# Kernel tuning notes

Hardware: AMD Instinct MI355X
Metric: run time of the kernel (lower is better)

The kernel has to match this reference:

```python
import jax, jax.numpy as jnp
import numpy as np

SEQ, B, OBS, H, MLP_H, ACT = 64, 8192, 47, 64, 32, 12


def setup_inputs() -> dict:
    key = jax.random.key(0)
    ks = jax.random.split(key, 10)
    s = 1.0 / np.sqrt(H)
    return {
        "obs_seq": jax.random.normal(ks[0], (SEQ, B, OBS), dtype=jnp.float32),
        "h0": jnp.zeros((1, B, H), jnp.float32),
        "c0": jnp.zeros((1, B, H), jnp.float32),
        "W_ih": jax.random.uniform(ks[1], (4 * H, OBS), jnp.float32, -s, s),
        "W_hh": jax.random.uniform(ks[2], (4 * H, H), jnp.float32, -s, s),
        "b_ih": jax.random.uniform(ks[3], (4 * H,), jnp.float32, -s, s),
        "b_hh": jax.random.uniform(ks[4], (4 * H,), jnp.float32, -s, s),
        "W1": jax.random.uniform(ks[5], (MLP_H, H), jnp.float32, -s, s),
        "b1": jax.random.uniform(ks[6], (MLP_H,), jnp.float32, -s, s),
        "W2": jax.random.uniform(ks[7], (ACT, MLP_H), jnp.float32, -0.1, 0.1),
        "b2": jnp.zeros((ACT,), jnp.float32),
        "masks": jax.random.randint(ks[8], (SEQ, B), 0, 2, dtype=jnp.int32),
    }


def _lstm_scan(obs_seq, h0, c0, W_ih, W_hh, b_ih, b_hh, masks):
    b = b_ih + b_hh

    def step(carry, inp):
        h, c = carry  # (B,H)
        x, m = inp
        m = m.astype(h.dtype)[:, None]  # (B,1): 0 resets hidden state
        h = h * m
        c = c * m
        gates = x @ W_ih.T + h @ W_hh.T + b  # (B,4H), torch order i,f,g,o
        i, f, g, o = jnp.split(gates, 4, axis=-1)
        c = jax.nn.sigmoid(f) * c + jax.nn.sigmoid(i) * jnp.tanh(g)
        h = jax.nn.sigmoid(o) * jnp.tanh(c)
        return (h, c), h

    (h, c), outs = jax.lax.scan(step, (h0[0], c0[0]), (obs_seq, masks))
    return outs, h, c


def reference(obs_seq, h0, c0, W_ih, W_hh, b_ih, b_hh, W1, b1, W2, b2, masks):
    lstm_out, h, c = _lstm_scan(obs_seq, h0, c0, W_ih, W_hh, b_ih, b_hh, masks)
    means = jax.nn.elu(lstm_out @ W1.T + b1) @ W2.T + b2  # (SEQ,B,ACT)
    return means, h[None], c[None]
```

## Files before the change

### kernel.cpp

```cpp
#include <hip/hip_runtime.h>
#include <hip/hip_bf16.h>

#define SEQ   64
#define BATCH 8192
#define OBS   47
#define HID   64
#define MLPH  32
#define ACT   12

#define BT 16
#define NT 512
#define NWG (BATCH / BT)

#define XS0O 0
#define XS1O 2048
#define HM0O 4096
#define HM1O 6144
#define XA0O 8192
#define XA1O 24576
#define M2OO 40960
#define MSKO 41984
#define W1LO 46080
#define W2LO 50176
#define SMEM_BYTES 51200

#define L2E  1.4426950408889634f
#define L2E2 2.8853900817779268f

typedef __attribute__((ext_vector_type(8))) short short8;
typedef __attribute__((ext_vector_type(4))) float f32x4;

__device__ __forceinline__ ushort f2bf(float f) {
  union { float f; unsigned u; } v; v.f = f;
  return (ushort)((v.u + 0x7FFFu + ((v.u >> 16) & 1u)) >> 16);
}
__device__ __forceinline__ float ex2(float x) {
#if __has_builtin(__builtin_amdgcn_exp2f)
  return __builtin_amdgcn_exp2f(x);
#else
  return __expf(x * 0.6931471805599453f);
#endif
}
__device__ __forceinline__ float rcpx(float x) {
#if __has_builtin(__builtin_amdgcn_rcpf)
  return __builtin_amdgcn_rcpf(x);
#else
  return __fdividef(1.0f, x);
#endif
}
__device__ __forceinline__ float sigf(float x)     { return rcpx(1.0f + ex2(-L2E * x)); }
__device__ __forceinline__ float tanhfast(float x) { return __builtin_fmaf(-2.0f, rcpx(1.0f + ex2(L2E2 * x)), 1.0f); }
__device__ __forceinline__ unsigned cvtpk(float lo, float hi) {
  unsigned r; asm("v_cvt_pk_bf16_f32 %0, %1, %2" : "=v"(r) : "v"(lo), "v"(hi)); return r;
}

__device__ __forceinline__ void barrier_lgkm() {
  __builtin_amdgcn_sched_barrier(0);
  asm volatile("s_waitcnt lgkmcnt(0)" ::: "memory");
  __builtin_amdgcn_s_barrier();
  __builtin_amdgcn_sched_barrier(0);
}

__device__ __forceinline__ int swz (int r, int ks) { return (r * 128 + ks * 2) ^ ((r & 7) << 4); }
__device__ __forceinline__ int swzM(int r, int cs) { return (r * 64  + cs * 2) ^ ((r & 7) << 4); }

extern "C" __global__ void __launch_bounds__(NT, 4)
lstm_policy(const float* __restrict__ obs, const float* __restrict__ h0,
            const float* __restrict__ c0, const float* __restrict__ Wih,
            const float* __restrict__ Whh, const float* __restrict__ bih,
            const float* __restrict__ bhh, const float* __restrict__ W1,
            const float* __restrict__ b1, const float* __restrict__ W2,
            const float* __restrict__ b2, const int* __restrict__ masks,
            float* __restrict__ out)
{
  __shared__ __align__(16) char sm[SMEM_BYTES];
  const int tid  = threadIdx.x;
  const int b0   = blockIdx.x * BT;
  const int lane = tid & 63;
  const int w    = tid >> 6;
  const int lr   = lane & 15;
  const int lg   = lane >> 4;
  const int j    = (w & 3) * 16 + lr;

  int xsl[4];
  #pragma unroll
  for (int nf = 0; nf < 4; ++nf)
    xsl[nf] = (j << 8) + ((((lg * 4 + nf) ^ lr) & 15) << 4);

  for (int idx = tid; idx < 256; idx += NT)
    *(f32x4*)(sm + idx * 16) = (f32x4){0.f, 0.f, 0.f, 0.f};
  for (int idx = tid; idx < SEQ * BT; idx += NT) {
    int t = idx >> 4, r = idx & 15;
    *(float*)(sm + MSKO + idx * 4) = (float)masks[t * BATCH + b0 + r];
  }
  if (tid < 64) {
    int l = tid, llr = l & 15, llg = l >> 4;
    #pragma unroll
    for (int tt = 0; tt < 2; ++tt)
      #pragma unroll
      for (int kk = 0; kk < 2; ++kk) {
        short8 f;
        const float* src = W1 + (tt * 16 + llr) * HID + kk * 32 + llg * 8;
        #pragma unroll
        for (int e = 0; e < 8; ++e) f[e] = (short)f2bf(src[e]);
        *(short8*)(sm + W1LO + ((tt * 2 + kk) * 64 + l) * 16) = f;
      }
    short8 f2;
    #pragma unroll
    for (int e = 0; e < 8; ++e)
      f2[e] = (llr < ACT) ? (short)f2bf(W2[llr * MLPH + llg * 8 + e]) : (short)0;
    *(short8*)(sm + W2LO + l * 16) = f2;
  }
  __syncthreads();

  short8 wf[4][2];
  float biasg[4] = {0, 0, 0, 0};
  float creg[4] = {0, 0, 0, 0}, hlast[4] = {0, 0, 0, 0};
  int shw[4];
  #pragma unroll
  for (int q = 0; q < 4; ++q) shw[q] = swz(lg * 4 + q, j);

  if (w < 4) {
    #pragma unroll
    for (int nf = 0; nf < 4; ++nf) {
      int n = nf * 64 + j;
      #pragma unroll
      for (int kk = 0; kk < 2; ++kk) {
        const float* src = Whh + n * HID + kk * 32 + lg * 8;
        short8 f;
        #pragma unroll
        for (int e = 0; e < 8; ++e) f[e] = (short)f2bf(src[e]);
        wf[nf][kk] = f;
      }
    }
    #pragma unroll
    for (int q = 0; q < 4; ++q) {
      int r = lg * 4 + q;
      creg[q] = c0[(size_t)(b0 + r) * HID + j];
      *(ushort*)(sm + HM0O + shw[q]) = f2bf(h0[(size_t)(b0 + r) * HID + j]);
    }
  } else {
    #pragma unroll
    for (int nf = 0; nf < 4; ++nf) {
      int n = nf * 64 + j;
      biasg[nf] = bih[n] + bhh[n];
      #pragma unroll
      for (int kk = 0; kk < 2; ++kk) {
        short8 f;
        #pragma unroll
        for (int e = 0; e < 8; ++e) {
          int k = kk * 32 + lg * 8 + e;
          f[e] = (k < OBS) ? (short)f2bf(Wih[n * OBS + k]) : (short)0;
        }
        wf[nf][kk] = f;
      }
    }
  }

  float b1v0 = 0.f, b1v1 = 0.f, b2v = 0.f;
  float* outp = out + ((size_t)(b0 + lg * 4)) * ACT + lr;
  if (w == 4) { b1v0 = b1[lr]; b1v1 = b1[16 + lr]; b2v = (lr < ACT) ? b2[lr] : 0.f; }

  const int oidx = tid - 320;
  const bool oact = (w >= 5) && (oidx >= 0) && (oidx < 188);
  int a_obs[4] = {0, 0, 0, 0};
  f32x4 ovh = {0.f, 0.f, 0.f, 0.f};
  const float* obsp = obs;
  if (oact) {
    #pragma unroll
    for (int e = 0; e < 4; ++e) {
      int flat = oidx * 4 + e;
      int r = flat / OBS, k = flat - OBS * r;
      a_obs[e] = swz(r, k);
    }
    f32x4 v0 = *(const f32x4*)(obs + (size_t)b0 * OBS + oidx * 4);
    f32x4 v1 = *(const f32x4*)(obs + ((size_t)BATCH + b0) * OBS + oidx * 4);
    #pragma unroll
    for (int e = 0; e < 4; ++e) *(ushort*)(sm + XS0O + a_obs[e]) = f2bf(v0[e]);
    #pragma unroll
    for (int e = 0; e < 4; ++e) *(ushort*)(sm + XS1O + a_obs[e]) = f2bf(v1[e]);
    obsp = obs + ((size_t)2 * BATCH + b0) * OBS + oidx * 4;
    ovh = *(const f32x4*)(obsp);
    obsp += (size_t)BATCH * OBS;
  }
  __syncthreads();

  auto do_xgemm = [&](int B) {
    const int xsb = B ? XS1O : XS0O;
    const int xab = B ? XA1O : XA0O;
    short8 ax0 = *(const short8*)(sm + xsb + swz(lr, lg * 8));
    short8 ax1 = *(const short8*)(sm + xsb + swz(lr, 32 + lg * 8));
    #pragma unroll
    for (int nf = 0; nf < 4; ++nf) {
      f32x4 a = (f32x4){biasg[nf], biasg[nf], biasg[nf], biasg[nf]};
      a = __builtin_amdgcn_mfma_f32_16x16x32_bf16(ax0, wf[nf][0], a, 0, 0, 0);
      a = __builtin_amdgcn_mfma_f32_16x16x32_bf16(ax1, wf[nf][1], a, 0, 0, 0);
      *(f32x4*)(sm + xab + xsl[nf]) = a;
    }
  };

  if (w >= 4) do_xgemm(0);
  __syncthreads();

  auto do_mlp = [&](int P) {
    const int hmb = P ? HM1O : HM0O;
    short8 hf0 = *(const short8*)(sm + hmb + swz(lr, lg * 8));
    short8 hf1 = *(const short8*)(sm + hmb + swz(lr, 32 + lg * 8));
    f32x4 am0 = (f32x4){b1v0, b1v0, b1v0, b1v0};
    f32x4 am1 = (f32x4){b1v1, b1v1, b1v1, b1v1};
    short8 wA;
    wA = *(const short8*)(sm + W1LO + (0 * 64 + lane) * 16);
    am0 = __builtin_amdgcn_mfma_f32_16x16x32_bf16(hf0, wA, am0, 0, 0, 0);
    wA = *(const short8*)(sm + W1LO + (1 * 64 + lane) * 16);
    am0 = __builtin_amdgcn_mfma_f32_16x16x32_bf16(hf1, wA, am0, 0, 0, 0);
    wA = *(const short8*)(sm + W1LO + (2 * 64 + lane) * 16);
    am1 = __builtin_amdgcn_mfma_f32_16x16x32_bf16(hf0, wA, am1, 0, 0, 0);
    wA = *(const short8*)(sm + W1LO + (3 * 64 + lane) * 16);
    am1 = __builtin_amdgcn_mfma_f32_16x16x32_bf16(hf1, wA, am1, 0, 0, 0);
    #pragma unroll
    for (int q = 0; q < 4; ++q) {
      int r = lg * 4 + q;
      float v0 = am0[q], v1 = am1[q];
      float e0 = v0 > 0.f ? v0 : (ex2(L2E * v0) - 1.f);
      float e1 = v1 > 0.f ? v1 : (ex2(L2E * v1) - 1.f);
      unsigned u = cvtpk(e0, e1);
      *(ushort*)(sm + M2OO + swzM(r, lr))      = (ushort)u;
      *(ushort*)(sm + M2OO + swzM(r, 16 + lr)) = (ushort)(u >> 16);
    }
    f32x4 a2 = (f32x4){b2v, b2v, b2v, b2v};
    short8 ef  = *(const short8*)(sm + M2OO + swzM(lr, lg * 8));
    short8 w2f = *(const short8*)(sm + W2LO + lane * 16);
    a2 = __builtin_amdgcn_mfma_f32_16x16x32_bf16(ef, w2f, a2, 0, 0, 0);
    if (lr < ACT) {
      #pragma unroll
      for (int q = 0; q < 4; ++q) outp[q * ACT] = a2[q];
    }
    outp += (size_t)BATCH * ACT;
  };

  auto do_step = [&](int P, int T) {
    if (w < 4) {
      __builtin_amdgcn_s_setprio(1);
      const int hmr = P ? HM1O : HM0O;
      const int hmw = P ? HM0O : HM1O;
      const int xar = P ? XA1O : XA0O;
      short8 ah0 = *(const short8*)(sm + hmr + swz(lr, lg * 8));
      short8 ah1 = *(const short8*)(sm + hmr + swz(lr, 32 + lg * 8));
      f32x4 xq0 = *(const f32x4*)(sm + xar + xsl[0]);
      f32x4 xq1 = *(const f32x4*)(sm + xar + xsl[1]);
      f32x4 xq2 = *(const f32x4*)(sm + xar + xsl[2]);
      f32x4 xq3 = *(const f32x4*)(sm + xar + xsl[3]);
      const f32x4 z = {0.f, 0.f, 0.f, 0.f};
      f32x4 pa0 = __builtin_amdgcn_mfma_f32_16x16x32_bf16(ah0, wf[0][0], z, 0, 0, 0);
      f32x4 pa1 = __builtin_amdgcn_mfma_f32_16x16x32_bf16(ah0, wf[1][0], z, 0, 0, 0);
      f32x4 pa2 = __builtin_amdgcn_mfma_f32_16x16x32_bf16(ah0, wf[2][0], z, 0, 0, 0);
      f32x4 pa3 = __builtin_amdgcn_mfma_f32_16x16x32_bf16(ah0, wf[3][0], z, 0, 0, 0);
      f32x4 pb0 = __builtin_amdgcn_mfma_f32_16x16x32_bf16(ah1, wf[0][1], z, 0, 0, 0);
      f32x4 pb1 = __builtin_amdgcn_mfma_f32_16x16x32_bf16(ah1, wf[1][1], z, 0, 0, 0);
      f32x4 pb2 = __builtin_amdgcn_mfma_f32_16x16x32_bf16(ah1, wf[2][1], z, 0, 0, 0);
      f32x4 pb3 = __builtin_amdgcn_mfma_f32_16x16x32_bf16(ah1, wf[3][1], z, 0, 0, 0);

      f32x4 mc = *(const f32x4*)(sm + MSKO + (T << 6) + (lg << 4));
      f32x4 g0 = xq0 + mc * (pa0 + pb0);
      f32x4 g1 = xq1 + mc * (pa1 + pb1);
      f32x4 g2 = xq2 + mc * (pa2 + pb2);
      f32x4 g3 = xq3 + mc * (pa3 + pb3);

      float hq[4];
      #pragma unroll
      for (int q = 0; q < 4; ++q) {
        float iv = sigf(g0[q]);
        float fv = sigf(g1[q]);
        float gv = tanhfast(g2[q]);
        float ov = sigf(g3[q]);
        float c  = fv * (creg[q] * mc[q]) + iv * gv;
        float h  = ov * tanhfast(c);
        creg[q]  = c;
        hlast[q] = h;
        hq[q]    = h;
      }
      unsigned u01 = cvtpk(hq[0], hq[1]);
      unsigned u23 = cvtpk(hq[2], hq[3]);
      *(ushort*)(sm + hmw + shw[0]) = (ushort)u01;
      *(ushort*)(sm + hmw + shw[1]) = (ushort)(u01 >> 16);
      *(ushort*)(sm + hmw + shw[2]) = (ushort)u23;
      *(ushort*)(sm + hmw + shw[3]) = (ushort)(u23 >> 16);
      __builtin_amdgcn_s_setprio(0);
    } else {
      if (T + 1 < SEQ) do_xgemm(P ^ 1);
      if (w == 4) {
        if (T > 0) do_mlp(P);
      } else if (oact) {
        f32x4 ovn = ovh;
        if (T + 3 < SEQ) { ovn = *(const f32x4*)(obsp); }
        obsp += (size_t)BATCH * OBS;
        if (T + 2 < SEQ) {
          const int xsw = P ? XS1O : XS0O;
          unsigned p0 = cvtpk(ovh[0], ovh[1]), p1 = cvtpk(ovh[2], ovh[3]);
          *(ushort*)(sm + xsw + a_obs[0]) = (ushort)p0;
          *(ushort*)(sm + xsw + a_obs[1]) = (ushort)(p0 >> 16);
          *(ushort*)(sm + xsw + a_obs[2]) = (ushort)p1;
          *(ushort*)(sm + xsw + a_obs[3]) = (ushort)(p1 >> 16);
        }
        ovh = ovn;
      }
    }
    barrier_lgkm();
  };

  for (int t = 0; t < SEQ; t += 2) {
    do_step(0, t);
    do_step(1, t + 1);
  }
  if (w == 4) do_mlp(0);

  if (w < 4) {
    float* hout = out + (size_t)SEQ * BATCH * ACT;
    float* cout = hout + (size_t)BATCH * HID;
    #pragma unroll
    for (int q = 0; q < 4; ++q) {
      int r = lg * 4 + q;
      hout[(size_t)(b0 + r) * HID + j] = hlast[q];
      cout[(size_t)(b0 + r) * HID + j] = creg[q];
    }
  }
}

extern "C" void kernel_launch(void* const* d_in, const int* in_sizes, int n_in,
                              void* d_out, int out_size, void* d_ws, size_t ws_size,
                              hipStream_t stream) {
  (void)in_sizes; (void)n_in; (void)d_ws; (void)ws_size; (void)out_size;
  lstm_policy<<<dim3(NWG), dim3(NT), 0, stream>>>(
      (const float*)d_in[0], (const float*)d_in[1], (const float*)d_in[2],
      (const float*)d_in[3], (const float*)d_in[4], (const float*)d_in[5],
      (const float*)d_in[6], (const float*)d_in[7], (const float*)d_in[8],
      (const float*)d_in[9], (const float*)d_in[10], (const int*)d_in[11],
      (float*)d_out);
}
```

Before: 97.95 us.

## Split MLP head across two waves with double-buffered ELU staging

The per-step MLP head is split into two stages: wave 4 computes the first layer plus ELU into a double-buffered LDS tile, and wave 5 runs the second layer and the global stores one step later. The aim is to shorten wave 4's per-step critical path so the helper waves stay ahead of the recurrent LSTM waves. It costs an extra 1KB of LDS, a wider pipeline skew, and an additional barrier in the epilogue. Wave 5 also keeps its obs-loading duties, so its work per step grows.

Measured after the change: 106.8 us. 9.0% more time.

```diff
diff --git a/kernel.cpp b/kernel.cpp
--- a/kernel.cpp
+++ b/kernel.cpp
@@ -18,11 +18,11 @@
 #define HM1O 6144
 #define XA0O 8192
 #define XA1O 24576
-#define M2OO 40960
-#define MSKO 41984
-#define W1LO 46080
-#define W2LO 50176
-#define SMEM_BYTES 51200
+#define M2EO 40960
+#define MSKO 43008
+#define W1LO 47104
+#define W2LO 51200
+#define SMEM_BYTES 52224
 
 #define L2E  1.4426950408889634f
 #define L2E2 2.8853900817779268f
@@ -158,8 +158,8 @@
   }
 
   float b1v0 = 0.f, b1v1 = 0.f, b2v = 0.f;
-  float* outp = out + ((size_t)(b0 + lg * 4)) * ACT + lr;
-  if (w == 4) { b1v0 = b1[lr]; b1v1 = b1[16 + lr]; b2v = (lr < ACT) ? b2[lr] : 0.f; }
+  if (w == 4) { b1v0 = b1[lr]; b1v1 = b1[16 + lr]; }
+  if (w == 5) { b2v = (lr < ACT) ? b2[lr] : 0.f; }
 
   const int oidx = tid - 320;
   const bool oact = (w >= 5) && (oidx >= 0) && (oidx < 188);
@@ -202,10 +202,10 @@
   if (w >= 4) do_xgemm(0);
   __syncthreads();
 
-  auto do_mlp = [&](int P) {
-    const int hmb = P ? HM1O : HM0O;
-    short8 hf0 = *(const short8*)(sm + hmb + swz(lr, lg * 8));
-    short8 hf1 = *(const short8*)(sm + hmb + swz(lr, 32 + lg * 8));
+  auto do_mlp1 = [&](int TT, int HMB) {
+    const int me = M2EO + (TT & 1) * 1024;
+    short8 hf0 = *(const short8*)(sm + HMB + swz(lr, lg * 8));
+    short8 hf1 = *(const short8*)(sm + HMB + swz(lr, 32 + lg * 8));
     f32x4 am0 = (f32x4){b1v0, b1v0, b1v0, b1v0};
     f32x4 am1 = (f32x4){b1v1, b1v1, b1v1, b1v1};
     short8 wA;
@@ -224,18 +224,22 @@
       float e0 = v0 > 0.f ? v0 : (ex2(L2E * v0) - 1.f);
       float e1 = v1 > 0.f ? v1 : (ex2(L2E * v1) - 1.f);
       unsigned u = cvtpk(e0, e1);
-      *(ushort*)(sm + M2OO + swzM(r, lr))      = (ushort)u;
-      *(ushort*)(sm + M2OO + swzM(r, 16 + lr)) = (ushort)(u >> 16);
-    }
+      *(ushort*)(sm + me + swzM(r, lr))      = (ushort)u;
+      *(ushort*)(sm + me + swzM(r, 16 + lr)) = (ushort)(u >> 16);
+    }
+  };
+
+  auto do_mlp2 = [&](int TT) {
+    const int me = M2EO + (TT & 1) * 1024;
     f32x4 a2 = (f32x4){b2v, b2v, b2v, b2v};
-    short8 ef  = *(const short8*)(sm + M2OO + swzM(lr, lg * 8));
+    short8 ef  = *(const short8*)(sm + me + swzM(lr, lg * 8));
     short8 w2f = *(const short8*)(sm + W2LO + lane * 16);
     a2 = __builtin_amdgcn_mfma_f32_16x16x32_bf16(ef, w2f, a2, 0, 0, 0);
     if (lr < ACT) {
-      #pragma unroll
-      for (int q = 0; q < 4; ++q) outp[q * ACT] = a2[q];
-    }
-    outp += (size_t)BATCH * ACT;
+      float* op = out + ((size_t)TT * BATCH + b0 + lg * 4) * ACT + lr;
+      #pragma unroll
+      for (int q = 0; q < 4; ++q) op[q * ACT] = a2[q];
+    }
   };
 
   auto do_step = [&](int P, int T) {
@@ -289,8 +293,11 @@
     } else {
       if (T + 1 < SEQ) do_xgemm(P ^ 1);
       if (w == 4) {
-        if (T > 0) do_mlp(P);
-      } else if (oact) {
+        if (T > 0) do_mlp1(T - 1, P ? HM1O : HM0O);
+      } else if (w == 5 && T > 1) {
+        do_mlp2(T - 2);
+      }
+      if (oact) {
         f32x4 ovn = ovh;
         if (T + 3 < SEQ) { ovn = *(const f32x4*)(obsp); }
         obsp += (size_t)BATCH * OBS;
@@ -312,7 +319,10 @@
     do_step(0, t);
     do_step(1, t + 1);
   }
-  if (w == 4) do_mlp(0);
+  if (w == 4) do_mlp1(63, HM0O);
+  else if (w == 5) do_mlp2(62);
+  barrier_lgkm();
+  if (w == 5) do_mlp2(63);
 
   if (w < 4) {
     float* hout = out + (size_t)SEQ * BATCH * ACT;
```
